# Kernel tuning notes

Measured on AMD Instinct MI355X. Metric: run time of the kernel, lower is better.

The kernel has to match this reference:

```python
import jax, jax.numpy as jnp
import numpy as np

B, H, W, R, C = 4, 64, 64, 64, 32  # batch, height, width, in-channels r, conv out-channels


def setup_inputs() -> dict:
    key = jax.random.key(0)
    kx, kf, kg = jax.random.split(key, 3)
    x = jax.random.normal(kx, (B, H, W, R), dtype=jnp.float32)
    # 1x1 conv with in_channels=1: kernel is effectively a length-C vector
    w_f = jax.random.normal(kf, (C,), dtype=jnp.float32) * 0.1
    w_g = jax.random.normal(kg, (C,), dtype=jnp.float32) * 0.1
    gamma = jnp.ones((), dtype=jnp.float32)
    return {"x": x, "w_f": w_f, "w_g": w_g, "gamma": gamma}


def reference(x, w_f, w_g, gamma):
    b, h, w, r = x.shape
    hw = h * w
    xs = x.reshape(b, hw, r)                      # [B, HW, R]
    # conv_f / conv_g: each scalar of xs times weight vector -> [B, HW, R*C]
    x_f = (xs[..., None] * w_f).reshape(b, hw, -1)
    x_g = (xs[..., None] * w_g).reshape(b, hw, -1)
    attn = jnp.einsum('bik,bjk->bij', x_f, x_g)   # [B, HW, HW]
    attn = jax.nn.softmax(attn, axis=-1) * gamma
    # out[b,j,r] = sum_i attn[b,j,i] * xs[b,i,r]
    out = jnp.einsum('bji,bir->bjr', attn, xs)
    return out.reshape(b, h, w, r)
```

## Files before the change

### kernel.cpp

```cpp
#include <hip/hip_runtime.h>


#define N_SEQ 4096
#define KS    8
#define LOG2E 1.4426950408889634f

typedef __attribute__((ext_vector_type(8))) short short8;
typedef __attribute__((ext_vector_type(4))) short short4v;
typedef __attribute__((ext_vector_type(4))) float f4;
typedef __attribute__((ext_vector_type(16))) float f32x16;
typedef _Float16 half8  __attribute__((ext_vector_type(8)));
typedef _Float16 half2t __attribute__((ext_vector_type(2)));
typedef __fp16   fp16x2 __attribute__((ext_vector_type(2)));

union U8  { short8 v8; short4v v4[2]; unsigned short u[8]; };
union PKU { fp16x2 f; half2t h; unsigned int u; };
union US  { short8 s; half8 h; };
union W4U { unsigned int u[4]; half8 h; };

#define MFMA16(a,b,c)  __builtin_amdgcn_mfma_f32_16x16x32_bf16(a,b,c,0,0,0)
#define MFMA32F(a,b,c) __builtin_amdgcn_mfma_f32_32x32x16_f16(a,b,c,0,0,0)

static __device__ __forceinline__ unsigned short f2bf(float f){
  unsigned int u = __float_as_uint(f);
  u += 0x7fffu + ((u>>16)&1u);
  return (unsigned short)(u>>16);
}
static __device__ __forceinline__ float bf2f(unsigned short b){
  return __uint_as_float(((unsigned int)b)<<16);
}
static __device__ __forceinline__ unsigned int pk_u32(float a, float b){
#if __has_builtin(__builtin_amdgcn_cvt_pkrtz)
  PKU u; u.f = __builtin_amdgcn_cvt_pkrtz(a, b); return u.u;
#else
  PKU u; u.h.x = (_Float16)a; u.h.y = (_Float16)b; return u.u;
#endif
}
static __device__ __forceinline__ float fexp2(float x){
#if __has_builtin(__builtin_amdgcn_exp2f)
  return __builtin_amdgcn_exp2f(x);
#else
  return exp2f(x);
#endif
}
static __device__ __forceinline__ f4 splat4(float v){ f4 r; r.x=v; r.y=v; r.z=v; r.w=v; return r; }
static __device__ __forceinline__ f4 exp2v(f4 v){
  f4 r; r.x=fexp2(v.x); r.y=fexp2(v.y); r.z=fexp2(v.z); r.w=fexp2(v.w); return r;
}
static __device__ __forceinline__ f4 max4(f4 a, f4 b){
  f4 r; r.x=fmaxf(a.x,b.x); r.y=fmaxf(a.y,b.y); r.z=fmaxf(a.z,b.z); r.w=fmaxf(a.w,b.w); return r;
}
static __device__ __forceinline__ f4 shx4(f4 v, int m){
  f4 r; r.x=__shfl_xor(v.x,m,64); r.y=__shfl_xor(v.y,m,64);
        r.z=__shfl_xor(v.z,m,64); r.w=__shfl_xor(v.w,m,64); return r;
}
static __device__ __forceinline__ f32x16 zero16(){
  f32x16 z;
  #pragma unroll
  for (int i = 0; i < 16; ++i) z[i] = 0.f;
  return z;
}
static __device__ __forceinline__ void gload16(const unsigned short* g, unsigned short* l){
  __builtin_amdgcn_global_load_lds((const __attribute__((address_space(1))) void*)g,
                                   (__attribute__((address_space(3))) void*)l, 16, 0, 0);
}
static __device__ __forceinline__ half8 mkfrag(unsigned int Da0, unsigned int Da1,
                                               unsigned int Db0, unsigned int Db1, bool hib){
  const unsigned int e0 = __shfl_xor(hib ? Da0 : Db0, 32, 64);
  const unsigned int e1 = __shfl_xor(hib ? Da1 : Db1, 32, 64);
  W4U w;
  w.u[0] = hib ? e0  : Da0;
  w.u[1] = hib ? e1  : Da1;
  w.u[2] = hib ? Db0 : e0;
  w.u[3] = hib ? Db1 : e1;
  return w.h;
}

__global__ __launch_bounds__(256) void prep6_kernel(
    const float* __restrict__ x,
    unsigned short* __restrict__ XF, unsigned short* __restrict__ VF)
{
  __shared__ __align__(16) unsigned short T [64][80];
  __shared__ __align__(16) unsigned short TT[64][80];
  const int tid  = threadIdx.x;
  const int bb   = blockIdx.x >> 6;
  const int tile = blockIdx.x & 63;
  {
    const int r  = tid >> 2;
    const int c4 = tid & 3;
    const float* src = x + ((size_t)(bb*N_SEQ + tile*64 + r))*64 + c4*16;
    unsigned short h[16];
    #pragma unroll
    for (int i = 0; i < 4; ++i) {
      const float4 f = *(const float4*)(src + i*4);
      const unsigned int u0 = pk_u32(f.x, f.y);
      const unsigned int u1 = pk_u32(f.z, f.w);
      h[i*4+0] = (unsigned short)(u0 & 0xffffu);
      h[i*4+1] = (unsigned short)(u0 >> 16);
      h[i*4+2] = (unsigned short)(u1 & 0xffffu);
      h[i*4+3] = (unsigned short)(u1 >> 16);
    }
    #pragma unroll
    for (int j = 0; j < 16; ++j) T[r][c4*16+j] = h[j];
    #pragma unroll
    for (int j = 0; j < 16; ++j) TT[c4*16+j][r] = h[j];
  }
  __syncthreads();
  const size_t ob = ((size_t)(bb*64 + tile)) * 4096;
  #pragma unroll
  for (int s0 = 0; s0 < 2; ++s0) {
    const int s  = s0*256 + tid;
    const int fb = s >> 6;
    const int l  = s & 63;
    const int rr = (fb >> 2)*32 + (l & 31);
    const int cc = (fb & 3)*16 + (l >> 5)*8;
    *(short8*)(XF + ob + (size_t)s*8) = *(const short8*)&T [rr][cc];
    *(short8*)(VF + ob + (size_t)s*8) = *(const short8*)&TT[rr][cc];
  }
}

__global__ __launch_bounds__(512, 2) void fattn6_kernel(
    const float* __restrict__ wf, const float* __restrict__ wg,
    const unsigned short* __restrict__ XF, const unsigned short* __restrict__ VF,
    float* __restrict__ OP, float* __restrict__ LP)
{
  __shared__ __align__(16) unsigned short KL[2][4096];
  __shared__ __align__(16) unsigned short VL[2][4096];

  const int tid  = threadIdx.x;
  const int lane = tid & 63;
  const int wv   = tid >> 6;
  const int l31  = lane & 31;
  const int hi   = lane >> 5;
  const bool hib = hi != 0;
  const int ks   = blockIdx.x >> 5;
  const int rem  = blockIdx.x & 31;
  const int bb   = rem >> 3;
  const int qB   = rem & 7;

  float s = 0.f;
  #pragma unroll
  for (int i = 0; i < 32; ++i) s += wf[i]*wg[i];
  const float s2 = s * LOG2E;
  const _Float16 s2h = (_Float16)s2;

  half8 qf[2][4];
  {
    const unsigned short* xq = XF + ((size_t)(bb*64 + qB*8 + wv))*4096 + lane*8;
    half8 sv;
    #pragma unroll
    for (int j = 0; j < 8; ++j) sv[j] = s2h;
    #pragma unroll
    for (int qg = 0; qg < 2; ++qg)
      #pragma unroll
      for (int kst = 0; kst < 4; ++kst) {
        US u; u.s = *(const short8*)(xq + (qg*4+kst)*512);
        qf[qg][kst] = u.h * sv;
      }
  }

  f32x16 Oc[2][2];
  #pragma unroll
  for (int qg = 0; qg < 2; ++qg)
    #pragma unroll
    for (int dg = 0; dg < 2; ++dg) Oc[qg][dg] = zero16();
  float lacc[2] = {0.f, 0.f};

  const unsigned short* gK = XF + ((size_t)(bb*64 + ks*8))*4096 + wv*512 + lane*8;
  const unsigned short* gV = VF + ((size_t)(bb*64 + ks*8))*4096 + wv*512 + lane*8;
  unsigned short* lK0 = &KL[0][wv*512];
  unsigned short* lV0 = &VL[0][wv*512];
  unsigned short* lK1 = &KL[1][wv*512];
  unsigned short* lV1 = &VL[1][wv*512];

  gload16(gK, lK0);
  gload16(gV, lV0);
  __syncthreads();

  #pragma unroll 1
  for (int it = 0; it < 8; ++it) {
    const int cur = it & 1;
    if (it + 1 < 8) {
      gload16(gK + (it+1)*4096, cur ? lK0 : lK1);
      gload16(gV + (it+1)*4096, cur ? lV0 : lV1);
    }
    const unsigned short* KB = &KL[cur][0];
    const unsigned short* VB = &VL[cur][0];

    #pragma unroll
    for (int kg = 0; kg < 2; ++kg) {
      half8 kf[4];
      #pragma unroll
      for (int kst = 0; kst < 4; ++kst) {
        US u; u.s = *(const short8*)(KB + ((kg*4+kst)*64 + lane)*8);
        kf[kst] = u.h;
      }
      f32x16 St[2];
      St[0] = zero16(); St[1] = zero16();
      __builtin_amdgcn_s_setprio(1);
      #pragma unroll
      for (int kst = 0; kst < 4; ++kst) {
        St[0] = MFMA32F(kf[kst], qf[0][kst], St[0]);
        St[1] = MFMA32F(kf[kst], qf[1][kst], St[1]);
      }
      __builtin_amdgcn_s_setprio(0);

      half8 pa[2][2];
      #pragma unroll
      for (int qg = 0; qg < 2; ++qg) {
        float p[16];
        float sm = 0.f;
        #pragma unroll
        for (int r = 0; r < 16; ++r) { p[r] = fexp2(St[qg][r]); sm += p[r]; }
        lacc[qg] += sm;
        const unsigned int D0 = pk_u32(p[0],  p[1]);
        const unsigned int D1 = pk_u32(p[2],  p[3]);
        const unsigned int D2 = pk_u32(p[4],  p[5]);
        const unsigned int D3 = pk_u32(p[6],  p[7]);
        const unsigned int D4 = pk_u32(p[8],  p[9]);
        const unsigned int D5 = pk_u32(p[10], p[11]);
        const unsigned int D6 = pk_u32(p[12], p[13]);
        const unsigned int D7 = pk_u32(p[14], p[15]);
        pa[qg][0] = mkfrag(D0, D1, D2, D3, hib);
        pa[qg][1] = mkfrag(D4, D5, D6, D7, hib);
      }

      __builtin_amdgcn_s_setprio(1);
      #pragma unroll
      for (int dg = 0; dg < 2; ++dg) {
        US v0, v1;
        v0.s = *(const short8*)(VB + ((dg*4 + kg*2 + 0)*64 + lane)*8);
        v1.s = *(const short8*)(VB + ((dg*4 + kg*2 + 1)*64 + lane)*8);
        #pragma unroll
        for (int qg = 0; qg < 2; ++qg) {
          Oc[qg][dg] = MFMA32F(pa[qg][0], v0.h, Oc[qg][dg]);
          Oc[qg][dg] = MFMA32F(pa[qg][1], v1.h, Oc[qg][dg]);
        }
      }
      __builtin_amdgcn_s_setprio(0);
    }
    __syncthreads();
  }

  lacc[0] += __shfl_xor(lacc[0], 32, 64);
  lacc[1] += __shfl_xor(lacc[1], 32, 64);

  float* op = OP + (size_t)blockIdx.x * (512*64);
  #pragma unroll
  for (int qg = 0; qg < 2; ++qg) {
    #pragma unroll
    for (int dg = 0; dg < 2; ++dg) {
      #pragma unroll
      for (int r = 0; r < 16; ++r) {
        const int row = wv*64 + qg*32 + (r & 3) + 8*(r >> 2) + 4*hi;
        op[row*64 + dg*32 + l31] = Oc[qg][dg][r];
      }
    }
    if (hi == 0)
      LP[(size_t)blockIdx.x*512 + wv*64 + qg*32 + l31] = lacc[qg];
  }
}

__global__ __launch_bounds__(256) void merge6_kernel(
    const float* __restrict__ OP, const float* __restrict__ LP,
    const float* __restrict__ gm, float* __restrict__ out)
{
  const int idx = blockIdx.x*256 + threadIdx.x;
  const int e0  = idx*4;
  const int d0  = e0 & 63;
  const int q   = e0 >> 6;
  const int bb  = q >> 12;
  const int qq  = q & 4095;
  const int qB  = qq >> 9;
  const int row = qq & 511;
  float4 acc = make_float4(0.f,0.f,0.f,0.f);
  float l = 0.f;
  #pragma unroll
  for (int sct = 0; sct < KS; ++sct) {
    const int blk = sct*32 + bb*8 + qB;
    const float4 o = *(const float4*)(OP + (size_t)blk*32768 + row*64 + d0);
    acc.x += o.x; acc.y += o.y; acc.z += o.z; acc.w += o.w;
    l += LP[(size_t)blk*512 + row];
  }
  const float w = gm[0] / l;
  float4 r; r.x = acc.x*w; r.y = acc.y*w; r.z = acc.z*w; r.w = acc.w*w;
  *(float4*)(out + e0) = r;
}

#define LDKF 72
#define TILEF (64*LDKF)
#define LDP 36

__global__ __launch_bounds__(256) void fattn_fallback(
    const float* __restrict__ x, const float* __restrict__ wf,
    const float* __restrict__ wg, const float* __restrict__ gm,
    float* __restrict__ out)
{
  __shared__ __align__(16) unsigned short KHI[2*TILEF];
  __shared__ __align__(16) unsigned short KLO[2*TILEF];
  __shared__ __align__(16) unsigned short VT [2*TILEF];
  __shared__ __align__(16) unsigned short PB [4*32*LDP];

  const int tid  = threadIdx.x;
  const int lane = tid & 63;
  const int wv   = tid >> 6;
  const int mg   = wv & 1;
  const int hh   = wv >> 1;
  const int quad = lane >> 4;
  const int l15  = lane & 15;
  const int bb   = blockIdx.x >> 6;
  const int qb   = (blockIdx.x & 63) << 6;

  float s = 0.f;
  #pragma unroll
  for (int i = 0; i < 32; ++i) s += wf[i]*wg[i];
  const float s2 = s * LOG2E;
  const float gamma = gm[0];

  const float* xb = x + ((size_t)bb * N_SEQ) * 64;

  short8 qhf[2][2], qlf[2][2];
  #pragma unroll
  for (int mt = 0; mt < 2; ++mt) {
    const int row = qb + mg*32 + mt*16 + l15;
    #pragma unroll
    for (int c = 0; c < 2; ++c) {
      const float* src = xb + row*64 + c*32 + quad*8;
      const float4 a0 = *(const float4*)src;
      const float4 a1 = *(const float4*)(src+4);
      float qv[8] = {a0.x,a0.y,a0.z,a0.w,a1.x,a1.y,a1.z,a1.w};
      U8 vh, vl;
      #pragma unroll
      for (int j = 0; j < 8; ++j) {
        float q = qv[j]*s2;
        unsigned short hb = f2bf(q);
        vh.u[j] = (short)hb;
        vl.u[j] = (short)f2bf(q - bf2f(hb));
      }
      qhf[mt][c] = vh.v8; qlf[mt][c] = vl.v8;
    }
  }

  f4 Oc[2][4], mo[2], ls[2];
  #pragma unroll
  for (int mt = 0; mt < 2; ++mt) {
    mo[mt] = splat4(-1e30f);
    ls[mt] = splat4(0.f);
    #pragma unroll
    for (int nt = 0; nt < 4; ++nt) Oc[mt][nt] = splat4(0.f);
  }

  const int sh   = tid >> 7;
  const int srow = (tid & 127) >> 1;
  const int sch  = tid & 1;

  float4 sr[8];
  {
    const float* sp = xb + (sh*2048 + srow)*64 + sch*32;
    #pragma unroll
    for (int i = 0; i < 8; ++i) sr[i] = *(const float4*)(sp + i*4);
    unsigned short hb[32], lb[32];
    #pragma unroll
    for (int i = 0; i < 8; ++i) {
      float vv[4] = {sr[i].x, sr[i].y, sr[i].z, sr[i].w};
      #pragma unroll
      for (int j = 0; j < 4; ++j) {
        unsigned short h = f2bf(vv[j]);
        hb[i*4+j] = h;
        lb[i*4+j] = f2bf(vv[j] - bf2f(h));
      }
    }
    const int kbase = sh*TILEF + srow*LDKF + sch*32;
    #pragma unroll
    for (int g = 0; g < 4; ++g) {
      U8 wh, wl;
      #pragma unroll
      for (int j = 0; j < 8; ++j) { wh.u[j]=(short)hb[g*8+j]; wl.u[j]=(short)lb[g*8+j]; }
      *(short8*)&KHI[kbase+g*8] = wh.v8;
      *(short8*)&KLO[kbase+g*8] = wl.v8;
    }
    #pragma unroll
    for (int j = 0; j < 32; ++j) VT[sh*TILEF + (sch*32+j)*LDKF + srow] = hb[j];
  }
  __syncthreads();

  #pragma unroll 1
  for (int t = 0; t < 32; ++t) {
    if (t+1 < 32) {
      const float* sp = xb + (sh*2048 + (t+1)*64 + srow)*64 + sch*32;
      #pragma unroll
      for (int i = 0; i < 8; ++i) sr[i] = *(const float4*)(sp + i*4);
    }

    f4 Sa[2][4];
    #pragma unroll
    for (int mt = 0; mt < 2; ++mt)
      #pragma unroll
      for (int n = 0; n < 4; ++n) Sa[mt][n] = splat4(0.f);

    const int kldsb = hh*TILEF;
    #pragma unroll
    for (int n = 0; n < 4; ++n) {
      #pragma unroll
      for (int c = 0; c < 2; ++c) {
        const int off = kldsb + (n*16 + l15)*LDKF + c*32 + quad*8;
        const short8 bh = *(const short8*)&KHI[off];
        const short8 bl = *(const short8*)&KLO[off];
        #pragma unroll
        for (int mt = 0; mt < 2; ++mt) {
          Sa[mt][n] = MFMA16(qhf[mt][c], bh, Sa[mt][n]);
          Sa[mt][n] = MFMA16(qlf[mt][c], bh, Sa[mt][n]);
          Sa[mt][n] = MFMA16(qhf[mt][c], bl, Sa[mt][n]);
        }
      }
    }

    f4 p[2][4];
    #pragma unroll
    for (int mt = 0; mt < 2; ++mt) {
      f4 rm = max4(max4(Sa[mt][0],Sa[mt][1]), max4(Sa[mt][2],Sa[mt][3]));
      rm = max4(rm, shx4(rm,1));
      rm = max4(rm, shx4(rm,2));
      rm = max4(rm, shx4(rm,4));
      rm = max4(rm, shx4(rm,8));
      f4 mn = max4(mo[mt], rm);
      f4 al = exp2v(mo[mt] - mn);
      mo[mt] = mn;
      f4 rs = splat4(0.f);
      #pragma unroll
      for (int n = 0; n < 4; ++n) { p[mt][n] = exp2v(Sa[mt][n] - mn); rs += p[mt][n]; }
      rs += shx4(rs,1); rs += shx4(rs,2); rs += shx4(rs,4); rs += shx4(rs,8);
      ls[mt] = ls[mt]*al + rs;
      #pragma unroll
      for (int nt = 0; nt < 4; ++nt) Oc[mt][nt] *= al;
    }

    const int pw = wv * (32*LDP);
    #pragma unroll
    for (int kc = 0; kc < 2; ++kc) {
      #pragma unroll
      for (int mt = 0; mt < 2; ++mt) {
        #pragma unroll
        for (int n2 = 0; n2 < 2; ++n2) {
          const f4 pv = p[mt][kc*2+n2];
          const int base = pw + (mt*16 + quad*4)*LDP + n2*16 + l15;
          ((unsigned short*)PB)[base        ] = f2bf(pv.x);
          ((unsigned short*)PB)[base +   LDP] = f2bf(pv.y);
          ((unsigned short*)PB)[base + 2*LDP] = f2bf(pv.z);
          ((unsigned short*)PB)[base + 3*LDP] = f2bf(pv.w);
        }
      }
      short8 pa[2];
      #pragma unroll
      for (int mt = 0; mt < 2; ++mt) {
        U8 u;
        const int rb = pw + (mt*16 + l15)*LDP + quad*8;
        u.v4[0] = *(const short4v*)&((unsigned short*)PB)[rb];
        u.v4[1] = *(const short4v*)&((unsigned short*)PB)[rb+4];
        pa[mt] = u.v8;
      }
      #pragma unroll
      for (int nt = 0; nt < 4; ++nt) {
        const short8 vb = *(const short8*)&VT[kldsb + (nt*16 + l15)*LDKF + kc*32 + quad*8];
        #pragma unroll
        for (int mt = 0; mt < 2; ++mt) Oc[mt][nt] = MFMA16(pa[mt], vb, Oc[mt][nt]);
      }
    }

    __syncthreads();

    if (t+1 < 32) {
      unsigned short hb[32], lb[32];
      #pragma unroll
      for (int i = 0; i < 8; ++i) {
        float vv[4] = {sr[i].x, sr[i].y, sr[i].z, sr[i].w};
        #pragma unroll
        for (int j = 0; j < 4; ++j) {
          unsigned short h = f2bf(vv[j]);
          hb[i*4+j] = h;
          lb[i*4+j] = f2bf(vv[j] - bf2f(h));
        }
      }
      const int kbase = sh*TILEF + srow*LDKF + sch*32;
      #pragma unroll
      for (int g = 0; g < 4; ++g) {
        U8 wh, wl;
        #pragma unroll
        for (int j = 0; j < 8; ++j) { wh.u[j]=(short)hb[g*8+j]; wl.u[j]=(short)lb[g*8+j]; }
        *(short8*)&KHI[kbase+g*8] = wh.v8;
        *(short8*)&KLO[kbase+g*8] = wl.v8;
      }
      #pragma unroll
      for (int j = 0; j < 32; ++j) VT[sh*TILEF + (sch*32+j)*LDKF + srow] = hb[j];
      __syncthreads();
    }
  }

  float* MO  = (float*)KHI;
  float* MML = (float*)KLO;
  if (hh == 1) {
    #pragma unroll
    for (int mt = 0; mt < 2; ++mt) {
      const int rbase = mg*32 + mt*16 + quad*4;
      #pragma unroll
      for (int nt = 0; nt < 4; ++nt) {
        MO[(rbase+0)*64 + nt*16 + l15] = Oc[mt][nt].x;
        MO[(rbase+1)*64 + nt*16 + l15] = Oc[mt][nt].y;
        MO[(rbase+2)*64 + nt*16 + l15] = Oc[mt][nt].z;
        MO[(rbase+3)*64 + nt*16 + l15] = Oc[mt][nt].w;
      }
      if (l15 == 0) {
        MML[rbase+0] = mo[mt].x; MML[rbase+1] = mo[mt].y;
        MML[rbase+2] = mo[mt].z; MML[rbase+3] = mo[mt].w;
        MML[64+rbase+0] = ls[mt].x; MML[64+rbase+1] = ls[mt].y;
        MML[64+rbase+2] = ls[mt].z; MML[64+rbase+3] = ls[mt].w;
      }
    }
  }
  __syncthreads();
  if (hh == 0) {
    #pragma unroll
    for (int mt = 0; mt < 2; ++mt) {
      const int rbase = mg*32 + mt*16 + quad*4;
      f4 m1, l1;
      m1.x = MML[rbase+0]; m1.y = MML[rbase+1]; m1.z = MML[rbase+2]; m1.w = MML[rbase+3];
      l1.x = MML[64+rbase+0]; l1.y = MML[64+rbase+1]; l1.z = MML[64+rbase+2]; l1.w = MML[64+rbase+3];
      const f4 mn = max4(mo[mt], m1);
      const f4 a0 = exp2v(mo[mt] - mn);
      const f4 a1 = exp2v(m1 - mn);
      f4 lt = ls[mt]*a0 + l1*a1;
      f4 w; w.x = gamma/lt.x; w.y = gamma/lt.y; w.z = gamma/lt.z; w.w = gamma/lt.w;
      #pragma unroll
      for (int nt = 0; nt < 4; ++nt) {
        #pragma unroll
        for (int rg = 0; rg < 4; ++rg) {
          const int rr = rbase + rg;
          const float o1 = MO[rr*64 + nt*16 + l15];
          const float val = (Oc[mt][nt][rg]*a0[rg] + o1*a1[rg]) * w[rg];
          out[((size_t)bb*N_SEQ + qb + rr)*64 + nt*16 + l15] = val;
        }
      }
    }
  }
}

extern "C" void kernel_launch(void* const* d_in, const int* in_sizes, int n_in,
                              void* d_out, int out_size, void* d_ws, size_t ws_size,
                              hipStream_t stream) {
  const float* x  = (const float*)d_in[0];
  const float* wf = (const float*)d_in[1];
  const float* wg = (const float*)d_in[2];
  const float* gm = (const float*)d_in[3];
  float* out = (float*)d_out;

  const size_t XF_OFF = 0;
  const size_t VF_OFF = 2097152;
  const size_t OP_OFF = 4194304;
  const size_t LP_OFF = OP_OFF + (size_t)256*512*64*4;
  const size_t NEED   = LP_OFF + (size_t)256*512*4;

  if (ws_size >= NEED) {
    unsigned short* XFp = (unsigned short*)((char*)d_ws + XF_OFF);
    unsigned short* VFp = (unsigned short*)((char*)d_ws + VF_OFF);
    float* OP = (float*)((char*)d_ws + OP_OFF);
    float* LP = (float*)((char*)d_ws + LP_OFF);
    prep6_kernel<<<dim3(256), dim3(256), 0, stream>>>(x, XFp, VFp);
    fattn6_kernel<<<dim3(256), dim3(512), 0, stream>>>(wf, wg, XFp, VFp, OP, LP);
    merge6_kernel<<<dim3(1024), dim3(256), 0, stream>>>(OP, LP, gm, out);
  } else {
    fattn_fallback<<<dim3(256), dim3(256), 0, stream>>>(x, wf, wg, gm, out);
  }
}
```

Before: 91.91 us.

## Halve attention block size to 4 waves and double grid, pad prep LDS

The attention kernel now uses 256-thread blocks covering 256 query rows each, with 512 blocks instead of 256 blocks of 512 threads. Each block cooperatively loads the shared K/V tiles with two 16-byte loads per thread, and the merge kernel and workspace layout are re-indexed to match. The prep kernel pads its LDS rows to 82 elements and reads them element by element, which changes bank mapping but gives up vectorised LDS reads. More blocks should improve CU occupancy and load balance, at the cost of each K/V tile being loaded by twice as many blocks.

```diff
diff --git a/kernel.cpp b/kernel.cpp
--- a/kernel.cpp
+++ b/kernel.cpp
@@ -80,8 +80,8 @@
     const float* __restrict__ x,
     unsigned short* __restrict__ XF, unsigned short* __restrict__ VF)
 {
-  __shared__ __align__(16) unsigned short T [64][80];
-  __shared__ __align__(16) unsigned short TT[64][80];
+  __shared__ __align__(16) unsigned short T [64][82];
+  __shared__ __align__(16) unsigned short TT[64][82];
   const int tid  = threadIdx.x;
   const int bb   = blockIdx.x >> 6;
   const int tile = blockIdx.x & 63;
@@ -114,12 +114,15 @@
     const int l  = s & 63;
     const int rr = (fb >> 2)*32 + (l & 31);
     const int cc = (fb & 3)*16 + (l >> 5)*8;
-    *(short8*)(XF + ob + (size_t)s*8) = *(const short8*)&T [rr][cc];
-    *(short8*)(VF + ob + (size_t)s*8) = *(const short8*)&TT[rr][cc];
-  }
-}
-
-__global__ __launch_bounds__(512, 2) void fattn6_kernel(
+    U8 a, b;
+    #pragma unroll
+    for (int j = 0; j < 8; ++j) { a.u[j] = T[rr][cc+j]; b.u[j] = TT[rr][cc+j]; }
+    *(short8*)(XF + ob + (size_t)s*8) = a.v8;
+    *(short8*)(VF + ob + (size_t)s*8) = b.v8;
+  }
+}
+
+__global__ __launch_bounds__(256, 2) void fattn8_kernel(
     const float* __restrict__ wf, const float* __restrict__ wg,
     const unsigned short* __restrict__ XF, const unsigned short* __restrict__ VF,
     float* __restrict__ OP, float* __restrict__ LP)
@@ -133,10 +136,10 @@
   const int l31  = lane & 31;
   const int hi   = lane >> 5;
   const bool hib = hi != 0;
-  const int ks   = blockIdx.x >> 5;
-  const int rem  = blockIdx.x & 31;
-  const int bb   = rem >> 3;
-  const int qB   = rem & 7;
+  const int ks   = blockIdx.x >> 6;
+  const int rem  = blockIdx.x & 63;
+  const int bb   = rem >> 4;
+  const int qP   = rem & 15;
 
   float s = 0.f;
   #pragma unroll
@@ -146,7 +149,7 @@
 
   half8 qf[2][4];
   {
-    const unsigned short* xq = XF + ((size_t)(bb*64 + qB*8 + wv))*4096 + lane*8;
+    const unsigned short* xq = XF + ((size_t)(bb*64 + qP*4 + wv))*4096 + lane*8;
     half8 sv;
     #pragma unroll
     for (int j = 0; j < 8; ++j) sv[j] = s2h;
@@ -166,23 +169,25 @@
     for (int dg = 0; dg < 2; ++dg) Oc[qg][dg] = zero16();
   float lacc[2] = {0.f, 0.f};
 
-  const unsigned short* gK = XF + ((size_t)(bb*64 + ks*8))*4096 + wv*512 + lane*8;
-  const unsigned short* gV = VF + ((size_t)(bb*64 + ks*8))*4096 + wv*512 + lane*8;
-  unsigned short* lK0 = &KL[0][wv*512];
-  unsigned short* lV0 = &VL[0][wv*512];
-  unsigned short* lK1 = &KL[1][wv*512];
-  unsigned short* lV1 = &VL[1][wv*512];
-
-  gload16(gK, lK0);
-  gload16(gV, lV0);
+  const unsigned short* gK = XF + ((size_t)(bb*64 + ks*8))*4096;
+  const unsigned short* gV = VF + ((size_t)(bb*64 + ks*8))*4096;
+
+  #pragma unroll
+  for (int c = 0; c < 2; ++c) {
+    gload16(gK + (c*256+tid)*8, &KL[0][(c*256+tid)*8]);
+    gload16(gV + (c*256+tid)*8, &VL[0][(c*256+tid)*8]);
+  }
   __syncthreads();
 
   #pragma unroll 1
   for (int it = 0; it < 8; ++it) {
     const int cur = it & 1;
     if (it + 1 < 8) {
-      gload16(gK + (it+1)*4096, cur ? lK0 : lK1);
-      gload16(gV + (it+1)*4096, cur ? lV0 : lV1);
+      #pragma unroll
+      for (int c = 0; c < 2; ++c) {
+        gload16(gK + (it+1)*4096 + (c*256+tid)*8, &KL[cur^1][(c*256+tid)*8]);
+        gload16(gV + (it+1)*4096 + (c*256+tid)*8, &VL[cur^1][(c*256+tid)*8]);
+      }
     }
     const unsigned short* KB = &KL[cur][0];
     const unsigned short* VB = &VL[cur][0];
@@ -245,7 +250,7 @@
   lacc[0] += __shfl_xor(lacc[0], 32, 64);
   lacc[1] += __shfl_xor(lacc[1], 32, 64);
 
-  float* op = OP + (size_t)blockIdx.x * (512*64);
+  float* op = OP + (size_t)blockIdx.x * (256*64);
   #pragma unroll
   for (int qg = 0; qg < 2; ++qg) {
     #pragma unroll
@@ -257,11 +262,11 @@
       }
     }
     if (hi == 0)
-      LP[(size_t)blockIdx.x*512 + wv*64 + qg*32 + l31] = lacc[qg];
-  }
-}
-
-__global__ __launch_bounds__(256) void merge6_kernel(
+      LP[(size_t)blockIdx.x*256 + wv*64 + qg*32 + l31] = lacc[qg];
+  }
+}
+
+__global__ __launch_bounds__(256) void merge8_kernel(
     const float* __restrict__ OP, const float* __restrict__ LP,
     const float* __restrict__ gm, float* __restrict__ out)
 {
@@ -271,16 +276,16 @@
   const int q   = e0 >> 6;
   const int bb  = q >> 12;
   const int qq  = q & 4095;
-  const int qB  = qq >> 9;
-  const int row = qq & 511;
+  const int qP  = qq >> 8;
+  const int row = qq & 255;
   float4 acc = make_float4(0.f,0.f,0.f,0.f);
   float l = 0.f;
   #pragma unroll
   for (int sct = 0; sct < KS; ++sct) {
-    const int blk = sct*32 + bb*8 + qB;
-    const float4 o = *(const float4*)(OP + (size_t)blk*32768 + row*64 + d0);
+    const int blk = sct*64 + bb*16 + qP;
+    const float4 o = *(const float4*)(OP + (size_t)blk*16384 + row*64 + d0);
     acc.x += o.x; acc.y += o.y; acc.z += o.z; acc.w += o.w;
-    l += LP[(size_t)blk*512 + row];
+    l += LP[(size_t)blk*256 + row];
   }
   const float w = gm[0] / l;
   float4 r; r.x = acc.x*w; r.y = acc.y*w; r.z = acc.z*w; r.w = acc.w*w;
@@ -556,8 +561,8 @@
   const size_t XF_OFF = 0;
   const size_t VF_OFF = 2097152;
   const size_t OP_OFF = 4194304;
-  const size_t LP_OFF = OP_OFF + (size_t)256*512*64*4;
-  const size_t NEED   = LP_OFF + (size_t)256*512*4;
+  const size_t LP_OFF = OP_OFF + (size_t)512*256*64*4;
+  const size_t NEED   = LP_OFF + (size_t)512*256*4;
 
   if (ws_size >= NEED) {
     unsigned short* XFp = (unsigned short*)((char*)d_ws + XF_OFF);
@@ -565,8 +570,8 @@
     float* OP = (float*)((char*)d_ws + OP_OFF);
     float* LP = (float*)((char*)d_ws + LP_OFF);
     prep6_kernel<<<dim3(256), dim3(256), 0, stream>>>(x, XFp, VFp);
-    fattn6_kernel<<<dim3(256), dim3(512), 0, stream>>>(wf, wg, XFp, VFp, OP, LP);
-    merge6_kernel<<<dim3(1024), dim3(256), 0, stream>>>(OP, LP, gm, out);
+    fattn8_kernel<<<dim3(512), dim3(256), 0, stream>>>(wf, wg, XFp, VFp, OP, LP);
+    merge8_kernel<<<dim3(1024), dim3(256), 0, stream>>>(OP, LP, gm, out);
   } else {
     fattn_fallback<<<dim3(256), dim3(256), 0, stream>>>(x, wf, wg, gm, out);
   }
```

Result: slower. 93.75 us (+2.0%).
